# Kernel optimization log

Measured on AMD Instinct MI355X. Metric: run time of the kernel, lower is better.

Reference implementation:

```python
import jax, jax.numpy as jnp
import numpy as np

D = 1024
H = 16
B = 8
N = 1024


def setup_inputs() -> dict:
    key = jax.random.key(0)
    k1, k2, k3 = jax.random.split(key, 3)
    x = jax.random.normal(k1, (B, N, D), dtype=jnp.float32)
    w_in = jax.random.normal(k2, (D, 3 * D), dtype=jnp.float32) * (1.0 / np.sqrt(D))
    w_out = jax.random.normal(k3, (D, D), dtype=jnp.float32) * (1.0 / np.sqrt(D))
    b_out = jnp.zeros((D,), dtype=jnp.float32)
    return {"x": x, "w_in": w_in, "w_out": w_out, "b_out": b_out}


def reference(x, w_in, w_out, b_out):
    h = H
    d = D // H
    scale = D ** (-0.5)  # note: full dimension, per source
    qkv = x @ w_in  # [B, N, 3D]
    # rearrange 'b n (qkv h d) -> qkv b h n d'
    qkv = qkv.reshape(x.shape[0], x.shape[1], 3, h, d)
    qkv = jnp.transpose(qkv, (2, 0, 3, 1, 4))
    q, k, v = qkv[0], qkv[1], qkv[2]
    scores = jnp.einsum('bhid,bhjd->bhij', q, k) * scale
    attn = jax.nn.softmax(scores, axis=-1)
    out = jnp.einsum('bhij,bhjd->bhid', attn, v)
    # 'b h n d -> b n (h d)'
    out = jnp.transpose(out, (0, 2, 1, 3)).reshape(x.shape[0], x.shape[1], h * d)
    return out @ w_out + b_out
```

## Files before the change

### kernel.cpp

```cpp
#include <hip/hip_runtime.h>
#include <stdint.h>
#include <stddef.h>

typedef __bf16 bf16;
typedef __bf16 bf16x4 __attribute__((ext_vector_type(4)));
typedef __bf16 bf16x8 __attribute__((ext_vector_type(8)));
typedef float  f32x4  __attribute__((ext_vector_type(4)));
typedef float  f32x16 __attribute__((ext_vector_type(16)));
typedef float  f32x4v __attribute__((ext_vector_type(4)));

__device__ __forceinline__ void gload_lds16(const void* g, void* lds) {
  __builtin_amdgcn_global_load_lds(
      (__attribute__((address_space(1))) void*)(uintptr_t)g,
      (__attribute__((address_space(3))) void*)lds,
      16, 0, 0);
}


__global__ void cvt_f32_to_bf16(const float* __restrict__ in, bf16* __restrict__ out, int n) {
  int i = (blockIdx.x * blockDim.x + threadIdx.x) * 4;
  if (i >= n) return;
  f32x4v v = *reinterpret_cast<const f32x4v*>(in + i);
  bf16x4 o;
  o[0] = (bf16)v[0]; o[1] = (bf16)v[1]; o[2] = (bf16)v[2]; o[3] = (bf16)v[3];
  *reinterpret_cast<bf16x4*>(out + i) = o;
}

__global__ void transpose_cvt(const float* __restrict__ in, bf16* __restrict__ out, int R, int C) {
  __shared__ bf16 tile[32][33];
  int c0 = blockIdx.x * 32, r0 = blockIdx.y * 32;
  int tx = threadIdx.x, ty = threadIdx.y;
  #pragma unroll
  for (int i = ty; i < 32; i += 8)
    tile[i][tx] = (bf16)in[(size_t)(r0 + i) * C + (c0 + tx)];
  __syncthreads();
  #pragma unroll
  for (int i = ty; i < 32; i += 8)
    out[(size_t)(c0 + i) * R + (r0 + tx)] = tile[tx][i];
}


template <typename OT, bool BIAS>
__global__ __launch_bounds__(256) void gemm_abt(
    const bf16* __restrict__ A,
    const bf16* __restrict__ Bt,
    const float* __restrict__ bias,
    OT* __restrict__ C, int M, int N, int K)
{
  __shared__ bf16 As[128 * 64];
  __shared__ bf16 Bs[128 * 64];

  const int tid = threadIdx.x;
  const int w = tid >> 6, l = tid & 63;
  const int l15 = l & 15, l4 = l >> 4, l7 = l & 7;
  const int wr = w >> 1, wc = w & 1;

  const int nwgx = N >> 7;
  const int nwg  = (M >> 7) * nwgx;
  const int cpx  = nwg >> 3;
  const int bid  = blockIdx.x;
  const int swz  = (bid & 7) * cpx + (bid >> 3);
  const int m0 = (swz / nwgx) * 128, n0 = (swz % nwgx) * 128;

  f32x4 acc[4][4];
  #pragma unroll
  for (int i = 0; i < 4; i++)
    #pragma unroll
    for (int j = 0; j < 4; j++) acc[i][j] = (f32x4){0.f, 0.f, 0.f, 0.f};

  const int srow  = w * 8 + (l >> 3);
  const int sslot = (l & 7) ^ ((l >> 3) & 7);
  const int KT = K >> 6;

  for (int kt = 0; kt < KT; ++kt) {
    __syncthreads();
    const int kcol = kt * 64 + sslot * 8;
    #pragma unroll
    for (int p = 0; p < 4; ++p) {
      gload_lds16(A  + (size_t)(m0 + p * 32 + srow) * K + kcol,
                  (char*)As + p * 4096 + w * 1024);
      gload_lds16(Bt + (size_t)(n0 + p * 32 + srow) * K + kcol,
                  (char*)Bs + p * 4096 + w * 1024);
    }
    __syncthreads();

    #pragma unroll
    for (int kk = 0; kk < 2; ++kk) {
      const int coff = (kk * 32 + l4 * 8) ^ (l7 << 3);
      bf16x8 af[4], bq[4];
      #pragma unroll
      for (int m = 0; m < 4; ++m) {
        int r = wr * 64 + m * 16 + l15;
        af[m] = *reinterpret_cast<const bf16x8*>(&As[r * 64 + coff]);
      }
      #pragma unroll
      for (int n = 0; n < 4; ++n) {
        int r = wc * 64 + n * 16 + l15;
        bq[n] = *reinterpret_cast<const bf16x8*>(&Bs[r * 64 + coff]);
      }
      #pragma unroll
      for (int m = 0; m < 4; ++m)
        #pragma unroll
        for (int n = 0; n < 4; ++n)
          acc[m][n] = __builtin_amdgcn_mfma_f32_16x16x32_bf16(af[m], bq[n], acc[m][n], 0, 0, 0);
    }
  }

  #pragma unroll
  for (int m = 0; m < 4; ++m) {
    #pragma unroll
    for (int n = 0; n < 4; ++n) {
      int col = n0 + wc * 64 + n * 16 + l15;
      float bv = BIAS ? bias[col] : 0.f;
      #pragma unroll
      for (int j = 0; j < 4; ++j) {
        int row = m0 + wr * 64 + m * 16 + l4 * 4 + j;
        float v = acc[m][n][j] + bv;
        C[(size_t)row * N + col] = (OT)v;
      }
    }
  }
}


__global__ __launch_bounds__(256) void attn_fused(
    const bf16* __restrict__ qkv,
    bf16* __restrict__ aout)
{
  __shared__ bf16 Ks[64 * 64];
  __shared__ bf16 Vt[64 * 64];
  __shared__ bf16 Pl[4][32 * 64];

  const int tid = threadIdx.x;
  const int w = tid >> 6, l = tid & 63;
  const int l31 = l & 31, hi = l >> 5;

  const int bid = blockIdx.x;
  const int c  = bid & 7, rr = bid >> 3;
  const int g  = c * 16 + (rr & 15);
  const int qt = rr >> 4;
  const int h  = g & 15;
  const int b  = g >> 4;

  const bf16* base = qkv + (size_t)b * 1024 * 3072;
  const int qrow0 = qt * 128 + w * 32;

  const float qscale = 0.03125f * 1.44269504f;
  bf16x8 qf[4];
  #pragma unroll
  for (int st = 0; st < 4; st++) {
    const bf16* p = base + (size_t)(qrow0 + l31) * 3072 + h * 64 + st * 16 + hi * 8;
    bf16x8 v = *reinterpret_cast<const bf16x8*>(p);
    #pragma unroll
    for (int e = 0; e < 8; e++) v[e] = (bf16)((float)v[e] * qscale);
    qf[st] = v;
  }

  bf16x8 onesf;
  #pragma unroll
  for (int e = 0; e < 8; e++) onesf[e] = (bf16)1.0f;

  f32x16 acc0 = {}, acc1 = {}, accS = {};

  const int skey  = w * 8 + (l >> 3);
  const int sslot = (l & 7) ^ ((l >> 3) & 7);
  const int vd0   = (tid & 15) * 4;
  const int vk0   = (tid >> 4) * 4;
  const int vslot = tid >> 5;
  const int vhalf = (tid >> 4) & 1;

  for (int kt = 0; kt < 16; ++kt) {
    __syncthreads();
    #pragma unroll
    for (int p = 0; p < 2; ++p)
      gload_lds16(base + (size_t)(kt * 64 + p * 32 + skey) * 3072 + 1024 + h * 64 + sslot * 8,
                  (char*)Ks + p * 4096 + w * 1024);
    {
      bf16x4 vv[4];
      #pragma unroll
      for (int i = 0; i < 4; ++i)
        vv[i] = *reinterpret_cast<const bf16x4*>(
            base + (size_t)(kt * 64 + vk0 + i) * 3072 + 2048 + h * 64 + vd0);
      #pragma unroll
      for (int j = 0; j < 4; ++j) {
        int d = vd0 + j;
        bf16x4 o; o[0] = vv[0][j]; o[1] = vv[1][j]; o[2] = vv[2][j]; o[3] = vv[3][j];
        *reinterpret_cast<bf16x4*>(
            &Vt[d * 64 + ((vslot ^ (d & 7) ^ ((d >> 3) & 7)) * 8 + vhalf * 4)]) = o;
      }
    }
    __syncthreads();

    #pragma unroll
    for (int ktile = 0; ktile < 2; ++ktile) {
      f32x16 s = {};
      const int key = ktile * 32 + l31;
      __builtin_amdgcn_s_setprio(1);
      #pragma unroll
      for (int st = 0; st < 4; ++st) {
        const int slot = (2 * st + hi) ^ (key & 7);
        bf16x8 kf = *reinterpret_cast<const bf16x8*>(&Ks[key * 64 + slot * 8]);
        s = __builtin_amdgcn_mfma_f32_32x32x16_bf16(kf, qf[st], s, 0, 0, 0);
      }
      __builtin_amdgcn_s_setprio(0);
      #pragma unroll
      for (int gq = 0; gq < 4; ++gq) {
        bf16x4 pb;
        #pragma unroll
        for (int j2 = 0; j2 < 4; ++j2) {
          float pv = __builtin_amdgcn_exp2f(s[4 * gq + j2]);
          pb[j2] = (bf16)pv;
        }
        const int chunk = ktile * 4 + gq;
        *reinterpret_cast<bf16x4*>(
            &Pl[w][l31 * 64 + ((chunk ^ (l31 & 7)) * 8 + hi * 4)]) = pb;
      }
    }

    const int d7x0 = (l31 & 7) ^ (l31 >> 3);
    const int d7x1 = d7x0 ^ 4;
    __builtin_amdgcn_s_setprio(1);
    #pragma unroll
    for (int st = 0; st < 4; ++st) {
      const int cs = 2 * st + hi;
      bf16x8 pa  = *reinterpret_cast<const bf16x8*>(
          &Pl[w][l31 * 64 + ((cs ^ (l31 & 7)) * 8)]);
      accS = __builtin_amdgcn_mfma_f32_32x32x16_bf16(pa, onesf, accS, 0, 0, 0);
      bf16x8 vf0 = *reinterpret_cast<const bf16x8*>(
          &Vt[l31 * 64 + ((cs ^ d7x0) * 8)]);
      acc0 = __builtin_amdgcn_mfma_f32_32x32x16_bf16(pa, vf0, acc0, 0, 0, 0);
      bf16x8 vf1 = *reinterpret_cast<const bf16x8*>(
          &Vt[(32 + l31) * 64 + ((cs ^ d7x1) * 8)]);
      acc1 = __builtin_amdgcn_mfma_f32_32x32x16_bf16(pa, vf1, acc1, 0, 0, 0);
    }
    __builtin_amdgcn_s_setprio(0);
  }

  #pragma unroll
  for (int reg = 0; reg < 16; ++reg) {
    int q_r = (reg & 3) + 8 * (reg >> 2) + 4 * hi;
    float rinv = 1.0f / accS[reg];
    size_t rowoff = ((size_t)b * 1024 + qrow0 + q_r) * 1024 + h * 64;
    aout[rowoff + l31]      = (bf16)(acc0[reg] * rinv);
    aout[rowoff + 32 + l31] = (bf16)(acc1[reg] * rinv);
  }
}


extern "C" void kernel_launch(void* const* d_in, const int* in_sizes, int n_in,
                              void* d_out, int out_size, void* d_ws, size_t ws_size,
                              hipStream_t stream) {
  const float* x     = (const float*)d_in[0];
  const float* w_in  = (const float*)d_in[1];
  const float* w_out = (const float*)d_in[2];
  const float* b_out = (const float*)d_in[3];
  float* out = (float*)d_out;

  bf16* xb    = (bf16*)d_ws;
  bf16* wint  = xb    + (size_t)8192 * 1024;
  bf16* woutt = wint  + (size_t)3072 * 1024;
  bf16* qkv   = woutt + (size_t)1024 * 1024;
  bf16* ao    = qkv   + (size_t)8192 * 3072;

  cvt_f32_to_bf16<<<8192, 256, 0, stream>>>(x, xb, 8192 * 1024);
  transpose_cvt<<<dim3(96, 32), dim3(32, 8), 0, stream>>>(w_in,  wint,  1024, 3072);
  transpose_cvt<<<dim3(32, 32), dim3(32, 8), 0, stream>>>(w_out, woutt, 1024, 1024);

  gemm_abt<bf16, false><<<1536, 256, 0, stream>>>(xb, wint, nullptr, qkv, 8192, 3072, 1024);

  attn_fused<<<1024, 256, 0, stream>>>(qkv, ao);

  gemm_abt<float, true><<<512, 256, 0, stream>>>(ao, woutt, b_out, out, 8192, 1024, 1024);
}
```

Baseline: 176.7 us.

## Switch GEMM to 32x32x16 MFMA tiles and drop setprio in attention

The GEMM inner loop now uses 32x32x16 bf16 MFMA with 2x2 accumulator tiles per wave instead of 16x16x32 with 4x4 tiles. This halves the LDS fragment reads per k-step and cuts the instruction count, and the epilogue is remapped to the 32x32 output layout. Separately, the s_setprio calls around the MFMA sections in the attention kernel are removed. The epilogue store pattern changes, with each lane writing 16 rows at a single column, which may alter write coalescing.

```diff
diff --git a/kernel.cpp b/kernel.cpp
--- a/kernel.cpp
+++ b/kernel.cpp
@@ -52,7 +52,7 @@
 
   const int tid = threadIdx.x;
   const int w = tid >> 6, l = tid & 63;
-  const int l15 = l & 15, l4 = l >> 4, l7 = l & 7;
+  const int l31 = l & 31, hi = l >> 5;
   const int wr = w >> 1, wc = w & 1;
 
   const int nwgx = N >> 7;
@@ -62,11 +62,11 @@
   const int swz  = (bid & 7) * cpx + (bid >> 3);
   const int m0 = (swz / nwgx) * 128, n0 = (swz % nwgx) * 128;
 
-  f32x4 acc[4][4];
-  #pragma unroll
-  for (int i = 0; i < 4; i++)
-    #pragma unroll
-    for (int j = 0; j < 4; j++) acc[i][j] = (f32x4){0.f, 0.f, 0.f, 0.f};
+  f32x16 acc[2][2];
+  #pragma unroll
+  for (int i = 0; i < 2; i++)
+    #pragma unroll
+    for (int j = 0; j < 2; j++) acc[i][j] = (f32x16){};
 
   const int srow  = w * 8 + (l >> 3);
   const int sslot = (l & 7) ^ ((l >> 3) & 7);
@@ -85,38 +85,37 @@
     __syncthreads();
 
     #pragma unroll
-    for (int kk = 0; kk < 2; ++kk) {
-      const int coff = (kk * 32 + l4 * 8) ^ (l7 << 3);
-      bf16x8 af[4], bq[4];
-      #pragma unroll
-      for (int m = 0; m < 4; ++m) {
-        int r = wr * 64 + m * 16 + l15;
-        af[m] = *reinterpret_cast<const bf16x8*>(&As[r * 64 + coff]);
-      }
-      #pragma unroll
-      for (int n = 0; n < 4; ++n) {
-        int r = wc * 64 + n * 16 + l15;
-        bq[n] = *reinterpret_cast<const bf16x8*>(&Bs[r * 64 + coff]);
-      }
-      #pragma unroll
-      for (int m = 0; m < 4; ++m)
+    for (int st = 0; st < 4; ++st) {
+      const int slot = (2 * st + hi) ^ (l31 & 7);
+      bf16x8 af[2], bq[2];
+      #pragma unroll
+      for (int mi = 0; mi < 2; ++mi) {
+        int row = wr * 64 + mi * 32 + l31;
+        af[mi] = *reinterpret_cast<const bf16x8*>(&As[row * 64 + slot * 8]);
+      }
+      #pragma unroll
+      for (int ni = 0; ni < 2; ++ni) {
+        int col = wc * 64 + ni * 32 + l31;
+        bq[ni] = *reinterpret_cast<const bf16x8*>(&Bs[col * 64 + slot * 8]);
+      }
+      #pragma unroll
+      for (int mi = 0; mi < 2; ++mi)
         #pragma unroll
-        for (int n = 0; n < 4; ++n)
-          acc[m][n] = __builtin_amdgcn_mfma_f32_16x16x32_bf16(af[m], bq[n], acc[m][n], 0, 0, 0);
-    }
-  }
-
-  #pragma unroll
-  for (int m = 0; m < 4; ++m) {
-    #pragma unroll
-    for (int n = 0; n < 4; ++n) {
-      int col = n0 + wc * 64 + n * 16 + l15;
-      float bv = BIAS ? bias[col] : 0.f;
-      #pragma unroll
-      for (int j = 0; j < 4; ++j) {
-        int row = m0 + wr * 64 + m * 16 + l4 * 4 + j;
-        float v = acc[m][n][j] + bv;
-        C[(size_t)row * N + col] = (OT)v;
+        for (int ni = 0; ni < 2; ++ni)
+          acc[mi][ni] = __builtin_amdgcn_mfma_f32_32x32x16_bf16(af[mi], bq[ni], acc[mi][ni], 0, 0, 0);
+    }
+  }
+
+  #pragma unroll
+  for (int ni = 0; ni < 2; ++ni) {
+    int col = n0 + wc * 64 + ni * 32 + l31;
+    float bv = BIAS ? bias[col] : 0.f;
+    #pragma unroll
+    for (int mi = 0; mi < 2; ++mi) {
+      #pragma unroll
+      for (int reg = 0; reg < 16; ++reg) {
+        int row = m0 + wr * 64 + mi * 32 + (reg & 3) + 8 * (reg >> 2) + 4 * hi;
+        C[(size_t)row * N + col] = (OT)(acc[mi][ni][reg] + bv);
       }
     }
   }
@@ -195,14 +194,12 @@
     for (int ktile = 0; ktile < 2; ++ktile) {
       f32x16 s = {};
       const int key = ktile * 32 + l31;
-      __builtin_amdgcn_s_setprio(1);
       #pragma unroll
       for (int st = 0; st < 4; ++st) {
         const int slot = (2 * st + hi) ^ (key & 7);
         bf16x8 kf = *reinterpret_cast<const bf16x8*>(&Ks[key * 64 + slot * 8]);
         s = __builtin_amdgcn_mfma_f32_32x32x16_bf16(kf, qf[st], s, 0, 0, 0);
       }
-      __builtin_amdgcn_s_setprio(0);
       #pragma unroll
       for (int gq = 0; gq < 4; ++gq) {
         bf16x4 pb;
@@ -219,7 +216,6 @@
 
     const int d7x0 = (l31 & 7) ^ (l31 >> 3);
     const int d7x1 = d7x0 ^ 4;
-    __builtin_amdgcn_s_setprio(1);
     #pragma unroll
     for (int st = 0; st < 4; ++st) {
       const int cs = 2 * st + hi;
@@ -233,7 +229,6 @@
           &Vt[(32 + l31) * 64 + ((cs ^ d7x1) * 8)]);
       acc1 = __builtin_amdgcn_mfma_f32_32x32x16_bf16(pa, vf1, acc1, 0, 0, 0);
     }
-    __builtin_amdgcn_s_setprio(0);
   }
 
   #pragma unroll
```

Result: faster. 170.6 us (-3.5%).
